# Kernel optimization log

Measured on AMD Instinct MI355X. Metric: run time of the kernel, lower is better.

Reference implementation:

```python
import jax, jax.numpy as jnp
import numpy as np

N_HEADS = 16
DIM_HEAD = 64
ROPE_THETA = 10000.0


def _rope_tables(seq_len, dim_head, dtype):
    # [N, dim_head//2] angle tables, llama-style interleaved-pair rotation
    inv_freq = 1.0 / (ROPE_THETA ** (jnp.arange(0, dim_head, 2, dtype=jnp.float32) / dim_head))
    t = jnp.arange(seq_len, dtype=jnp.float32)
    freqs = jnp.outer(t, inv_freq)  # [N, D/2]
    return jnp.cos(freqs).astype(dtype), jnp.sin(freqs).astype(dtype)


def _apply_rope(x, cos, sin):
    # x: [B, H, N, D]; rotate interleaved pairs (x[2i], x[2i+1])
    xr = x[..., 0::2]
    xi = x[..., 1::2]
    cos = cos[None, None, :, :]
    sin = sin[None, None, :, :]
    out_r = xr * cos - xi * sin
    out_i = xr * sin + xi * cos
    return jnp.stack([out_r, out_i], axis=-1).reshape(x.shape)


def _l2norm(x, eps=1e-12):
    return x / jnp.maximum(jnp.linalg.norm(x, axis=-1, keepdims=True), eps)


def setup_inputs() -> dict:
    key = jax.random.key(0)
    ks = jax.random.split(key, 5)
    B, N, dim = 1, 4096, N_HEADS * DIM_HEAD
    q = jax.random.normal(ks[0], (B, N, dim), dtype=jnp.float32)
    k = jax.random.normal(ks[1], (B, N, dim), dtype=jnp.float32)
    v = jax.random.normal(ks[2], (B, N, dim), dtype=jnp.float32)
    qk_scale = jnp.full((1, 1, 1, DIM_HEAD), 10.0, dtype=jnp.float32)
    w_out = jax.random.normal(ks[3], (dim, dim), dtype=jnp.float32) * (dim ** -0.5)
    b_out = jnp.zeros((dim,), dtype=jnp.float32)
    return {"q": q, "k": k, "v": v, "qk_scale": qk_scale, "w_out": w_out, "b_out": b_out}


def reference(q, k, v, qk_scale, w_out, b_out):
    B, N, dim = q.shape
    H, D = N_HEADS, DIM_HEAD
    scale = D ** -0.5
    # [B, N, dim] -> [B, H, N, D]
    q = q.reshape(B, N, H, D).transpose(0, 2, 1, 3)
    k = k.reshape(B, N, H, D).transpose(0, 2, 1, 3)
    v = v.reshape(B, N, H, D).transpose(0, 2, 1, 3)
    # RoPE
    cos, sin = _rope_tables(N, D, q.dtype)
    q = _apply_rope(q, cos, sin)
    k = _apply_rope(k, cos, sin)
    # QK-norm: L2-normalize then learned scale
    q = _l2norm(q) * qk_scale
    k = _l2norm(k) * qk_scale
    # explicit attention (non-flash)
    scores = jnp.einsum('bhid,bhjd->bhij', q, k) * scale
    probs = jax.nn.softmax(scores, axis=-1)
    out = jnp.einsum('bhij,bhjd->bhid', probs, v)
    out = out.transpose(0, 2, 1, 3).reshape(B, N, dim)
    # Linear: y = x W^T + b
    return out @ w_out.T + b_out
```

## Files before the change

kernel.cpp:

```cpp
#include <hip/hip_runtime.h>
#include <hip/hip_bf16.h>

#define N_CTX 4096
#define NH    16
#define DH    64
#define DIM   1024
#define NSPLIT 4
#define KT_PER_SPLIT (N_CTX / 64 / NSPLIT)

typedef __attribute__((ext_vector_type(8))) short bf16x8;
typedef __attribute__((ext_vector_type(4))) float f32x4;
typedef __attribute__((ext_vector_type(2))) unsigned u32x2;

__device__ __forceinline__ ushort f2bf(float f) {
    union { float f; unsigned u; } x; x.f = f;
    unsigned r = (x.u + 0x7FFFu + ((x.u >> 16) & 1u)) >> 16;
    return (ushort)r;
}
__device__ __forceinline__ float bf2f(ushort u) {
    union { unsigned u; float f; } x; x.u = ((unsigned)u) << 16; return x.f;
}
__device__ __forceinline__ unsigned fbits(float f) {
    union { float f; unsigned u; } x; x.f = f; return x.u;
}
__device__ __forceinline__ unsigned pack_bf16(float lo, float hi) {
    unsigned a = fbits(lo) + 0x8000u;
    unsigned b = fbits(hi) + 0x8000u;
#if defined(__has_builtin)
#if __has_builtin(__builtin_amdgcn_perm)
    return __builtin_amdgcn_perm(b, a, 0x07060302u);
#else
    return (a >> 16) | (b & 0xFFFF0000u);
#endif
#else
    return (a >> 16) | (b & 0xFFFF0000u);
#endif
}
__device__ __forceinline__ float fast_exp2(float x) {
#if defined(__has_builtin)
#if __has_builtin(__builtin_amdgcn_exp2f)
    return __builtin_amdgcn_exp2f(x);
#else
    return exp2f(x);
#endif
#else
    return exp2f(x);
#endif
}
__device__ __forceinline__ void fast_sincos(float ang, float* s, float* c) {
#if defined(__has_builtin)
#if __has_builtin(__builtin_amdgcn_sinf) && __has_builtin(__builtin_amdgcn_cosf) && __has_builtin(__builtin_amdgcn_fractf)
    float rev = __builtin_amdgcn_fractf(ang * 0.15915494309189535f);
    *s = __builtin_amdgcn_sinf(rev);
    *c = __builtin_amdgcn_cosf(rev);
    return;
#endif
#endif
    sincosf(ang, s, c);
}

__device__ __forceinline__ void pl32_swap(unsigned &a, unsigned &b) {
#if defined(__has_builtin)
#if __has_builtin(__builtin_amdgcn_permlane32_swap)
    u32x2 r = __builtin_amdgcn_permlane32_swap(a, b, false, false);
    a = r[0]; b = r[1];
    return;
#endif
#endif
    const int lane = (int)(threadIdx.x & 63);
    unsigned ax = (unsigned)__shfl_xor((int)a, 32, 64);
    unsigned bx = (unsigned)__shfl_xor((int)b, 32, 64);
    unsigned na = (lane & 32) ? bx : a;
    unsigned nb = (lane & 32) ? b  : ax;
    a = na; b = nb;
}
__device__ __forceinline__ void pl16_swap(unsigned &a, unsigned &b) {
#if defined(__has_builtin)
#if __has_builtin(__builtin_amdgcn_permlane16_swap)
    u32x2 r = __builtin_amdgcn_permlane16_swap(a, b, false, false);
    a = r[0]; b = r[1];
    return;
#endif
#endif
    const int lane = (int)(threadIdx.x & 63);
    unsigned ax = (unsigned)__shfl_xor((int)a, 16, 64);
    unsigned bx = (unsigned)__shfl_xor((int)b, 16, 64);
    unsigned na = (lane & 16) ? bx : a;
    unsigned nb = (lane & 16) ? b  : ax;
    a = na; b = nb;
}

#define SC 0.18033688011112042f
#define LF 0.4152410118609203f

__global__ __launch_bounds__(256) void prep_kernel(
    const float* __restrict__ qg, const float* __restrict__ kg,
    const float* __restrict__ qk_scale,
    ushort* __restrict__ qb, ushort* __restrict__ kb)
{
    const int lane = threadIdx.x & 63;
    const int wave = threadIdx.x >> 6;
    const int row  = blockIdx.x * 4 + wave;
    const int n = row >> 4;
    const int h = row & 15;
    const int isk = blockIdx.y;
    const float* __restrict__ x = isk ? kg : qg;
    ushort* __restrict__ xb = isk ? kb : qb;
    const float premul = isk ? 1.0f : SC;

    float val = x[(size_t)n * DIM + h * DH + lane];
    float other = __shfl_xor(val, 1, 64);

    const int i = lane >> 1;
    float inv_freq = fast_exp2((float)i * -LF);
    float ang = (float)n * inv_freq;
    float s, c;
    fast_sincos(ang, &s, &c);

    float r = (lane & 1) ? fmaf(other, s, val * c)
                         : fmaf(val, c, -(other * s));

    float ss = r * r;
    #pragma unroll
    for (int off = 32; off > 0; off >>= 1)
        ss += __shfl_xor(ss, off, 64);
    float invn = rsqrtf(fmaxf(ss, 1e-24f));
    float scl  = qk_scale[lane] * premul;

    xb[((size_t)h * N_CTX + n) * DH + lane] = f2bf(r * invn * scl);
}

__global__ __launch_bounds__(256) void vtrans_kernel(
    const float* __restrict__ v, ushort* __restrict__ vt)
{
    __shared__ ushort L[64][68];
    const int kt = blockIdx.x, h = blockIdx.y, t = threadIdx.x;

    for (int e = t; e < 4096; e += 256) {
        int key = e >> 6, d = e & 63;
        float f = v[(size_t)(kt * 64 + key) * DIM + h * DH + d];
        L[d][key] = f2bf(f);
    }
    __syncthreads();
    for (int e = t; e < 4096; e += 256) {
        int d = e >> 6, key = e & 63;
        vt[((size_t)h * DH + d) * N_CTX + kt * 64 + key] = L[d][key];
    }
}

__global__ __launch_bounds__(256) void wconv_kernel(
    const float* __restrict__ w, ushort* __restrict__ wb)
{
    int i = (blockIdx.x * 256 + threadIdx.x) * 4;
    float4 f = *(const float4*)&w[i];
    ushort4 u;
    u.x = f2bf(f.x); u.y = f2bf(f.y); u.z = f2bf(f.z); u.w = f2bf(f.w);
    *(ushort4*)&wb[i] = u;
}

__global__ __launch_bounds__(256) void attn_kernel(
    const ushort* __restrict__ qb, const ushort* __restrict__ kb,
    const ushort* __restrict__ vt, ushort* __restrict__ opart,
    float* __restrict__ lpart)
{
    __shared__ ushort Ks[2][64][72];
    __shared__ ushort Vt[2][64][72];

    const int h     = blockIdx.y;
    const int qbase = blockIdx.x * 128;
    const int sp    = blockIdx.z;
    const int kbase = sp * (N_CTX / NSPLIT);
    const int t    = threadIdx.x;
    const int w    = t >> 6;
    const int lane = t & 63;
    const int l15  = lane & 15;
    const int quad = lane >> 4;

    bf16x8 qf[2][2];
    #pragma unroll
    for (int qt = 0; qt < 2; qt++) {
        const size_t qrow = ((size_t)h * N_CTX + qbase + w * 32 + qt * 16 + l15) * DH;
        qf[qt][0] = *(const bf16x8*)&qb[qrow + quad * 8];
        qf[qt][1] = *(const bf16x8*)&qb[qrow + 32 + quad * 8];
    }

    float l_part[2] = {0.0f, 0.0f};
    f32x4 o_acc[4][2];
    #pragma unroll
    for (int dt = 0; dt < 4; dt++)
        #pragma unroll
        for (int qt = 0; qt < 2; qt++)
            o_acc[dt][qt] = (f32x4){0.f, 0.f, 0.f, 0.f};

    const int sr = t >> 3;
    const int sc = (t & 7) * 8;
    const ushort* kp0 = &kb[((size_t)h * N_CTX + kbase + sr) * DH + sc];
    const ushort* kp1 = kp0 + (size_t)32 * DH;
    const ushort* vp0 = &vt[((size_t)h * DH + sr) * N_CTX + kbase + sc];
    const ushort* vp1 = vp0 + (size_t)32 * N_CTX;

    bf16x8 kr0 = *(const bf16x8*)kp0, kr1 = *(const bf16x8*)kp1;
    bf16x8 vr0 = *(const bf16x8*)vp0, vr1 = *(const bf16x8*)vp1;
    kp0 += (size_t)64 * DH; kp1 += (size_t)64 * DH;
    vp0 += 64;              vp1 += 64;
    *(bf16x8*)&Ks[0][sr][sc]      = kr0;
    *(bf16x8*)&Ks[0][sr + 32][sc] = kr1;
    *(bf16x8*)&Vt[0][sr][sc]      = vr0;
    *(bf16x8*)&Vt[0][sr + 32][sc] = vr1;
    __syncthreads();

    for (int kt = 0; kt < KT_PER_SPLIT; kt++) {
        const int cur = kt & 1;
        const bool more = (kt + 1 < KT_PER_SPLIT);
        if (more) {
            kr0 = *(const bf16x8*)kp0;  kp0 += (size_t)64 * DH;
            kr1 = *(const bf16x8*)kp1;  kp1 += (size_t)64 * DH;
            vr0 = *(const bf16x8*)vp0;  vp0 += 64;
            vr1 = *(const bf16x8*)vp1;  vp1 += 64;
        }

        #pragma unroll
        for (int jp = 0; jp < 2; jp++) {
            unsigned pa[2][2], pb[2][2];
            #pragma unroll
            for (int jj = 0; jj < 2; jj++) {
                const int j = jp * 2 + jj;
                bf16x8 kf0 = *(const bf16x8*)&Ks[cur][j * 16 + l15][quad * 8];
                bf16x8 kf1 = *(const bf16x8*)&Ks[cur][j * 16 + l15][32 + quad * 8];
                f32x4 s0 = (f32x4){0.f, 0.f, 0.f, 0.f};
                f32x4 s1 = (f32x4){0.f, 0.f, 0.f, 0.f};
                s0 = __builtin_amdgcn_mfma_f32_16x16x32_bf16(kf0, qf[0][0], s0, 0, 0, 0);
                s1 = __builtin_amdgcn_mfma_f32_16x16x32_bf16(kf0, qf[1][0], s1, 0, 0, 0);
                s0 = __builtin_amdgcn_mfma_f32_16x16x32_bf16(kf1, qf[0][1], s0, 0, 0, 0);
                s1 = __builtin_amdgcn_mfma_f32_16x16x32_bf16(kf1, qf[1][1], s1, 0, 0, 0);

                {
                    float p0 = fast_exp2(s0.x), p1 = fast_exp2(s0.y);
                    float p2 = fast_exp2(s0.z), p3 = fast_exp2(s0.w);
                    l_part[0] += (p0 + p1) + (p2 + p3);
                    unsigned d0 = pack_bf16(p0, p1), d1 = pack_bf16(p2, p3);
                    if (jj == 0) { pa[0][0] = d0; pa[0][1] = d1; }
                    else         { pb[0][0] = d0; pb[0][1] = d1; }
                }
                {
                    float p0 = fast_exp2(s1.x), p1 = fast_exp2(s1.y);
                    float p2 = fast_exp2(s1.z), p3 = fast_exp2(s1.w);
                    l_part[1] += (p0 + p1) + (p2 + p3);
                    unsigned d0 = pack_bf16(p0, p1), d1 = pack_bf16(p2, p3);
                    if (jj == 0) { pa[1][0] = d0; pa[1][1] = d1; }
                    else         { pb[1][0] = d0; pb[1][1] = d1; }
                }
            }

            bf16x8 pw[2];
            #pragma unroll
            for (int qt = 0; qt < 2; qt++) {
                unsigned x0 = pa[qt][0], y0 = pb[qt][0];
                unsigned x1 = pa[qt][1], y1 = pb[qt][1];
                pl32_swap(x0, y0);
                pl32_swap(x1, y1);
                pl16_swap(x0, y0);
                pl16_swap(x1, y1);
                uint4 wd; wd.x = x0; wd.y = x1; wd.z = y0; wd.w = y1;
                pw[qt] = __builtin_bit_cast(bf16x8, wd);
            }

            #pragma unroll
            for (int dt = 0; dt < 4; dt++) {
                bf16x8 vf = *(const bf16x8*)&Vt[cur][dt * 16 + l15][jp * 32 + quad * 8];
                o_acc[dt][0] = __builtin_amdgcn_mfma_f32_16x16x32_bf16(vf, pw[0], o_acc[dt][0], 0, 0, 0);
                o_acc[dt][1] = __builtin_amdgcn_mfma_f32_16x16x32_bf16(vf, pw[1], o_acc[dt][1], 0, 0, 0);
            }
        }

        if (more) {
            *(bf16x8*)&Ks[cur ^ 1][sr][sc]      = kr0;
            *(bf16x8*)&Ks[cur ^ 1][sr + 32][sc] = kr1;
            *(bf16x8*)&Vt[cur ^ 1][sr][sc]      = vr0;
            *(bf16x8*)&Vt[cur ^ 1][sr + 32][sc] = vr1;
            __syncthreads();
        }
    }

    #pragma unroll
    for (int qt = 0; qt < 2; qt++) {
        float v = l_part[qt];
        v += __shfl_xor(v, 16, 64);
        v += __shfl_xor(v, 32, 64);
        if (quad == 0)
            lpart[(size_t)sp * NH * N_CTX + (size_t)h * N_CTX
                  + qbase + w * 32 + qt * 16 + l15] = v;
    }

    #pragma unroll
    for (int qt = 0; qt < 2; qt++)
        #pragma unroll
        for (int dt = 0; dt < 4; dt++) {
            f32x4 o = o_acc[dt][qt];
            ushort4 ov;
            ov.x = f2bf(o.x); ov.y = f2bf(o.y);
            ov.z = f2bf(o.z); ov.w = f2bf(o.w);
            *(ushort4*)&opart[((size_t)sp * N_CTX + qbase + w * 32 + qt * 16 + l15) * DIM
                              + h * DH + dt * 16 + quad * 4] = ov;
        }
}

__global__ __launch_bounds__(256) void combine_kernel(
    const ushort* __restrict__ opart, const float* __restrict__ lpart,
    ushort* __restrict__ attnb)
{
    const int idx = blockIdx.x * 256 + threadIdx.x;
    const int n   = idx >> 8;
    const int rem = idx & 255;
    const int h   = rem >> 4;
    const size_t e = (size_t)n * DIM + h * DH + (rem & 15) * 4;

    float s0 = 0.f, s1 = 0.f, s2 = 0.f, s3 = 0.f, lsum = 0.f;
    #pragma unroll
    for (int sp = 0; sp < NSPLIT; sp++) {
        ushort4 u = *(const ushort4*)&opart[(size_t)sp * N_CTX * DIM + e];
        s0 += bf2f(u.x); s1 += bf2f(u.y); s2 += bf2f(u.z); s3 += bf2f(u.w);
        lsum += lpart[(size_t)sp * NH * N_CTX + (size_t)h * N_CTX + n];
    }
    float li = 1.0f / lsum;

    ushort4 r;
    r.x = f2bf(s0 * li); r.y = f2bf(s1 * li);
    r.z = f2bf(s2 * li); r.w = f2bf(s3 * li);
    *(ushort4*)&attnb[e] = r;
}

__global__ __launch_bounds__(256) void proj_kernel(
    const ushort* __restrict__ A, const ushort* __restrict__ W,
    const float* __restrict__ bias, float* __restrict__ out)
{
    __shared__ ushort As[2][64][72];
    __shared__ ushort Ws[2][64][72];

    const int nbase = blockIdx.x * 64;
    const int obase = blockIdx.y * 64;
    const int t    = threadIdx.x;
    const int w    = t >> 6;
    const int lane = t & 63;
    const int l15  = lane & 15;
    const int quad = lane >> 4;
    const int rw   = (w >> 1) * 32;
    const int cw   = (w & 1) * 32;

    f32x4 acc[2][2];
    #pragma unroll
    for (int mt = 0; mt < 2; mt++)
        #pragma unroll
        for (int nt = 0; nt < 2; nt++)
            acc[mt][nt] = (f32x4){0.f, 0.f, 0.f, 0.f};

    const int sr = t >> 3;
    const int sc = (t & 7) * 8;
    const ushort* ap0 = &A[(size_t)(nbase + sr) * DIM + sc];
    const ushort* ap1 = ap0 + (size_t)32 * DIM;
    const ushort* wp0 = &W[(size_t)(obase + sr) * DIM + sc];
    const ushort* wp1 = wp0 + (size_t)32 * DIM;

    bf16x8 ar0 = *(const bf16x8*)ap0, ar1 = *(const bf16x8*)ap1;
    bf16x8 wr0 = *(const bf16x8*)wp0, wr1 = *(const bf16x8*)wp1;
    ap0 += 64; ap1 += 64; wp0 += 64; wp1 += 64;
    *(bf16x8*)&As[0][sr][sc]      = ar0;
    *(bf16x8*)&As[0][sr + 32][sc] = ar1;
    *(bf16x8*)&Ws[0][sr][sc]      = wr0;
    *(bf16x8*)&Ws[0][sr + 32][sc] = wr1;
    __syncthreads();

    for (int kt = 0; kt < DIM / 64; kt++) {
        const int cur = kt & 1;
        const bool more = (kt + 1 < DIM / 64);
        if (more) {
            ar0 = *(const bf16x8*)ap0;  ap0 += 64;
            ar1 = *(const bf16x8*)ap1;  ap1 += 64;
            wr0 = *(const bf16x8*)wp0;  wp0 += 64;
            wr1 = *(const bf16x8*)wp1;  wp1 += 64;
        }

        bf16x8 af[2][2], bfr[2][2];
        #pragma unroll
        for (int mt = 0; mt < 2; mt++)
            #pragma unroll
            for (int kh = 0; kh < 2; kh++)
                af[mt][kh] = *(const bf16x8*)&As[cur][rw + mt * 16 + l15][kh * 32 + quad * 8];
        #pragma unroll
        for (int nt = 0; nt < 2; nt++)
            #pragma unroll
            for (int kh = 0; kh < 2; kh++)
                bfr[nt][kh] = *(const bf16x8*)&Ws[cur][cw + nt * 16 + l15][kh * 32 + quad * 8];

        #pragma unroll
        for (int mt = 0; mt < 2; mt++)
            #pragma unroll
            for (int nt = 0; nt < 2; nt++) {
                acc[mt][nt] = __builtin_amdgcn_mfma_f32_16x16x32_bf16(af[mt][0], bfr[nt][0], acc[mt][nt], 0, 0, 0);
                acc[mt][nt] = __builtin_amdgcn_mfma_f32_16x16x32_bf16(af[mt][1], bfr[nt][1], acc[mt][nt], 0, 0, 0);
            }

        if (more) {
            *(bf16x8*)&As[cur ^ 1][sr][sc]      = ar0;
            *(bf16x8*)&As[cur ^ 1][sr + 32][sc] = ar1;
            *(bf16x8*)&Ws[cur ^ 1][sr][sc]      = wr0;
            *(bf16x8*)&Ws[cur ^ 1][sr + 32][sc] = wr1;
            __syncthreads();
        }
    }

    #pragma unroll
    for (int nt = 0; nt < 2; nt++) {
        int o = obase + cw + nt * 16 + l15;
        float bb = bias[o];
        #pragma unroll
        for (int mt = 0; mt < 2; mt++) {
            int nrow = nbase + rw + mt * 16 + quad * 4;
            out[(size_t)(nrow + 0) * DIM + o] = acc[mt][nt].x + bb;
            out[(size_t)(nrow + 1) * DIM + o] = acc[mt][nt].y + bb;
            out[(size_t)(nrow + 2) * DIM + o] = acc[mt][nt].z + bb;
            out[(size_t)(nrow + 3) * DIM + o] = acc[mt][nt].w + bb;
        }
    }
}

extern "C" void kernel_launch(void* const* d_in, const int* in_sizes, int n_in,
                              void* d_out, int out_size, void* d_ws, size_t ws_size,
                              hipStream_t stream)
{
    const float* q        = (const float*)d_in[0];
    const float* k        = (const float*)d_in[1];
    const float* v        = (const float*)d_in[2];
    const float* qk_scale = (const float*)d_in[3];
    const float* w_out    = (const float*)d_in[4];
    const float* b_out    = (const float*)d_in[5];
    float* out = (float*)d_out;

    const size_t per = (size_t)NH * N_CTX * DH;
    ushort* qb    = (ushort*)d_ws;
    ushort* kb    = qb + per;
    ushort* vtg   = kb + per;
    ushort* attnb = vtg + per;
    ushort* wb    = attnb + per;
    ushort* opart = wb + (size_t)DIM * DIM;
    float*  lpart = (float*)(opart + (size_t)NSPLIT * N_CTX * DIM);

    prep_kernel<<<dim3(N_CTX * NH / 4, 2), 256, 0, stream>>>(q, k, qk_scale, qb, kb);
    vtrans_kernel<<<dim3(N_CTX / 64, NH), 256, 0, stream>>>(v, vtg);
    wconv_kernel<<<dim3(DIM * DIM / 1024), 256, 0, stream>>>(w_out, wb);
    attn_kernel<<<dim3(N_CTX / 128, NH, NSPLIT), 256, 0, stream>>>(qb, kb, vtg, opart, lpart);
    combine_kernel<<<dim3(N_CTX * DIM / 4 / 256), 256, 0, stream>>>(opart, lpart, attnb);
    proj_kernel<<<dim3(N_CTX / 64, DIM / 64), 256, 0, stream>>>(attnb, wb, b_out, out);
}
```

Measured before the change: 241.0 us.

## Double attention Q tile per block, single-buffer K/V smem, precompute RoPE tables

```diff
diff --git a/kernel.cpp b/kernel.cpp
--- a/kernel.cpp
+++ b/kernel.cpp
@@ -93,9 +93,21 @@
 #define SC 0.18033688011112042f
 #define LF 0.4152410118609203f
 
+__global__ __launch_bounds__(256) void rope_table_kernel(
+    float* __restrict__ ct, float* __restrict__ st)
+{
+    const int idx = blockIdx.x * 256 + threadIdx.x;
+    const int n = idx >> 5, i = idx & 31;
+    float inv_freq = fast_exp2((float)i * -LF);
+    float s, c;
+    fast_sincos((float)n * inv_freq, &s, &c);
+    ct[idx] = c; st[idx] = s;
+}
+
 __global__ __launch_bounds__(256) void prep_kernel(
     const float* __restrict__ qg, const float* __restrict__ kg,
     const float* __restrict__ qk_scale,
+    const float* __restrict__ ct, const float* __restrict__ st,
     ushort* __restrict__ qb, ushort* __restrict__ kb)
 {
     const int lane = threadIdx.x & 63;
@@ -112,10 +124,8 @@
     float other = __shfl_xor(val, 1, 64);
 
     const int i = lane >> 1;
-    float inv_freq = fast_exp2((float)i * -LF);
-    float ang = (float)n * inv_freq;
-    float s, c;
-    fast_sincos(ang, &s, &c);
+    const float c = ct[(n << 5) | i];
+    const float s = st[(n << 5) | i];
 
     float r = (lane & 1) ? fmaf(other, s, val * c)
                          : fmaf(val, c, -(other * s));
@@ -163,11 +173,11 @@
     const ushort* __restrict__ vt, ushort* __restrict__ opart,
     float* __restrict__ lpart)
 {
-    __shared__ ushort Ks[2][64][72];
-    __shared__ ushort Vt[2][64][72];
+    __shared__ ushort Ks[64][72];
+    __shared__ ushort Vt[64][72];
 
     const int h     = blockIdx.y;
-    const int qbase = blockIdx.x * 128;
+    const int qbase = blockIdx.x * 256;
     const int sp    = blockIdx.z;
     const int kbase = sp * (N_CTX / NSPLIT);
     const int t    = threadIdx.x;
@@ -176,20 +186,20 @@
     const int l15  = lane & 15;
     const int quad = lane >> 4;
 
-    bf16x8 qf[2][2];
-    #pragma unroll
-    for (int qt = 0; qt < 2; qt++) {
-        const size_t qrow = ((size_t)h * N_CTX + qbase + w * 32 + qt * 16 + l15) * DH;
+    bf16x8 qf[4][2];
+    #pragma unroll
+    for (int qt = 0; qt < 4; qt++) {
+        const size_t qrow = ((size_t)h * N_CTX + qbase + w * 64 + qt * 16 + l15) * DH;
         qf[qt][0] = *(const bf16x8*)&qb[qrow + quad * 8];
         qf[qt][1] = *(const bf16x8*)&qb[qrow + 32 + quad * 8];
     }
 
-    float l_part[2] = {0.0f, 0.0f};
-    f32x4 o_acc[4][2];
+    float l_part[4] = {0.f, 0.f, 0.f, 0.f};
+    f32x4 o_acc[4][4];
     #pragma unroll
     for (int dt = 0; dt < 4; dt++)
         #pragma unroll
-        for (int qt = 0; qt < 2; qt++)
+        for (int qt = 0; qt < 4; qt++)
             o_acc[dt][qt] = (f32x4){0.f, 0.f, 0.f, 0.f};
 
     const int sr = t >> 3;
@@ -198,63 +208,56 @@
     const ushort* kp1 = kp0 + (size_t)32 * DH;
     const ushort* vp0 = &vt[((size_t)h * DH + sr) * N_CTX + kbase + sc];
     const ushort* vp1 = vp0 + (size_t)32 * N_CTX;
-
     bf16x8 kr0 = *(const bf16x8*)kp0, kr1 = *(const bf16x8*)kp1;
     bf16x8 vr0 = *(const bf16x8*)vp0, vr1 = *(const bf16x8*)vp1;
-    kp0 += (size_t)64 * DH; kp1 += (size_t)64 * DH;
-    vp0 += 64;              vp1 += 64;
-    *(bf16x8*)&Ks[0][sr][sc]      = kr0;
-    *(bf16x8*)&Ks[0][sr + 32][sc] = kr1;
-    *(bf16x8*)&Vt[0][sr][sc]      = vr0;
-    *(bf16x8*)&Vt[0][sr + 32][sc] = vr1;
-    __syncthreads();
 
     for (int kt = 0; kt < KT_PER_SPLIT; kt++) {
-        const int cur = kt & 1;
-        const bool more = (kt + 1 < KT_PER_SPLIT);
-        if (more) {
-            kr0 = *(const bf16x8*)kp0;  kp0 += (size_t)64 * DH;
-            kr1 = *(const bf16x8*)kp1;  kp1 += (size_t)64 * DH;
-            vr0 = *(const bf16x8*)vp0;  vp0 += 64;
-            vr1 = *(const bf16x8*)vp1;  vp1 += 64;
+        __syncthreads();
+        *(bf16x8*)&Ks[sr][sc]      = kr0;
+        *(bf16x8*)&Ks[sr + 32][sc] = kr1;
+        *(bf16x8*)&Vt[sr][sc]      = vr0;
+        *(bf16x8*)&Vt[sr + 32][sc] = vr1;
+        __syncthreads();
+        if (kt + 1 < KT_PER_SPLIT) {
+            kr0 = *(const bf16x8*)(kp0 + (size_t)(kt + 1) * 64 * DH);
+            kr1 = *(const bf16x8*)(kp1 + (size_t)(kt + 1) * 64 * DH);
+            vr0 = *(const bf16x8*)(vp0 + (size_t)(kt + 1) * 64);
+            vr1 = *(const bf16x8*)(vp1 + (size_t)(kt + 1) * 64);
         }
 
         #pragma unroll
         for (int jp = 0; jp < 2; jp++) {
-            unsigned pa[2][2], pb[2][2];
+            unsigned pa[4][2], pb[4][2];
             #pragma unroll
             for (int jj = 0; jj < 2; jj++) {
                 const int j = jp * 2 + jj;
-                bf16x8 kf0 = *(const bf16x8*)&Ks[cur][j * 16 + l15][quad * 8];
-                bf16x8 kf1 = *(const bf16x8*)&Ks[cur][j * 16 + l15][32 + quad * 8];
-                f32x4 s0 = (f32x4){0.f, 0.f, 0.f, 0.f};
-                f32x4 s1 = (f32x4){0.f, 0.f, 0.f, 0.f};
-                s0 = __builtin_amdgcn_mfma_f32_16x16x32_bf16(kf0, qf[0][0], s0, 0, 0, 0);
-                s1 = __builtin_amdgcn_mfma_f32_16x16x32_bf16(kf0, qf[1][0], s1, 0, 0, 0);
-                s0 = __builtin_amdgcn_mfma_f32_16x16x32_bf16(kf1, qf[0][1], s0, 0, 0, 0);
-                s1 = __builtin_amdgcn_mfma_f32_16x16x32_bf16(kf1, qf[1][1], s1, 0, 0, 0);
-
-                {
-                    float p0 = fast_exp2(s0.x), p1 = fast_exp2(s0.y);
-                    float p2 = fast_exp2(s0.z), p3 = fast_exp2(s0.w);
-                    l_part[0] += (p0 + p1) + (p2 + p3);
+                bf16x8 kf0 = *(const bf16x8*)&Ks[j * 16 + l15][quad * 8];
+                bf16x8 kf1 = *(const bf16x8*)&Ks[j * 16 + l15][32 + quad * 8];
+                f32x4 sv[4];
+                #pragma unroll
+                for (int qt = 0; qt < 4; qt++)
+                    sv[qt] = (f32x4){0.f, 0.f, 0.f, 0.f};
+                #pragma unroll
+                for (int qt = 0; qt < 4; qt++)
+                    sv[qt] = __builtin_amdgcn_mfma_f32_16x16x32_bf16(kf0, qf[qt][0], sv[qt], 0, 0, 0);
+                #pragma unroll
+                for (int qt = 0; qt < 4; qt++)
+                    sv[qt] = __builtin_amdgcn_mfma_f32_16x16x32_bf16(kf1, qf[qt][1], sv[qt], 0, 0, 0);
+
+                #pragma unroll
+                for (int qt = 0; qt < 4; qt++) {
+                    float p0 = fast_exp2(sv[qt].x), p1 = fast_exp2(sv[qt].y);
+                    float p2 = fast_exp2(sv[qt].z), p3 = fast_exp2(sv[qt].w);
+                    l_part[qt] += (p0 + p1) + (p2 + p3);
                     unsigned d0 = pack_bf16(p0, p1), d1 = pack_bf16(p2, p3);
-                    if (jj == 0) { pa[0][0] = d0; pa[0][1] = d1; }
-                    else         { pb[0][0] = d0; pb[0][1] = d1; }
-                }
-                {
-                    float p0 = fast_exp2(s1.x), p1 = fast_exp2(s1.y);
-                    float p2 = fast_exp2(s1.z), p3 = fast_exp2(s1.w);
-                    l_part[1] += (p0 + p1) + (p2 + p3);
-                    unsigned d0 = pack_bf16(p0, p1), d1 = pack_bf16(p2, p3);
-                    if (jj == 0) { pa[1][0] = d0; pa[1][1] = d1; }
-                    else         { pb[1][0] = d0; pb[1][1] = d1; }
+                    if (jj == 0) { pa[qt][0] = d0; pa[qt][1] = d1; }
+                    else         { pb[qt][0] = d0; pb[qt][1] = d1; }
                 }
             }
 
-            bf16x8 pw[2];
-            #pragma unroll
-            for (int qt = 0; qt < 2; qt++) {
+            bf16x8 pw[4];
+            #pragma unroll
+            for (int qt = 0; qt < 4; qt++) {
                 unsigned x0 = pa[qt][0], y0 = pb[qt][0];
                 unsigned x1 = pa[qt][1], y1 = pb[qt][1];
                 pl32_swap(x0, y0);
@@ -267,40 +270,33 @@
 
             #pragma unroll
             for (int dt = 0; dt < 4; dt++) {
-                bf16x8 vf = *(const bf16x8*)&Vt[cur][dt * 16 + l15][jp * 32 + quad * 8];
-                o_acc[dt][0] = __builtin_amdgcn_mfma_f32_16x16x32_bf16(vf, pw[0], o_acc[dt][0], 0, 0, 0);
-                o_acc[dt][1] = __builtin_amdgcn_mfma_f32_16x16x32_bf16(vf, pw[1], o_acc[dt][1], 0, 0, 0);
+                bf16x8 vf = *(const bf16x8*)&Vt[dt * 16 + l15][jp * 32 + quad * 8];
+                #pragma unroll
+                for (int qt = 0; qt < 4; qt++)
+                    o_acc[dt][qt] = __builtin_amdgcn_mfma_f32_16x16x32_bf16(vf, pw[qt], o_acc[dt][qt], 0, 0, 0);
             }
         }
-
-        if (more) {
-            *(bf16x8*)&Ks[cur ^ 1][sr][sc]      = kr0;
-            *(bf16x8*)&Ks[cur ^ 1][sr + 32][sc] = kr1;
-            *(bf16x8*)&Vt[cur ^ 1][sr][sc]      = vr0;
-            *(bf16x8*)&Vt[cur ^ 1][sr + 32][sc] = vr1;
-            __syncthreads();
-        }
-    }
-
-    #pragma unroll
-    for (int qt = 0; qt < 2; qt++) {
+    }
+
+    #pragma unroll
+    for (int qt = 0; qt < 4; qt++) {
         float v = l_part[qt];
         v += __shfl_xor(v, 16, 64);
         v += __shfl_xor(v, 32, 64);
         if (quad == 0)
             lpart[(size_t)sp * NH * N_CTX + (size_t)h * N_CTX
-                  + qbase + w * 32 + qt * 16 + l15] = v;
-    }
-
-    #pragma unroll
-    for (int qt = 0; qt < 2; qt++)
+                  + qbase + w * 64 + qt * 16 + l15] = v;
+    }
+
+    #pragma unroll
+    for (int qt = 0; qt < 4; qt++)
         #pragma unroll
         for (int dt = 0; dt < 4; dt++) {
             f32x4 o = o_acc[dt][qt];
             ushort4 ov;
             ov.x = f2bf(o.x); ov.y = f2bf(o.y);
             ov.z = f2bf(o.z); ov.w = f2bf(o.w);
-            *(ushort4*)&opart[((size_t)sp * N_CTX + qbase + w * 32 + qt * 16 + l15) * DIM
+            *(ushort4*)&opart[((size_t)sp * N_CTX + qbase + w * 64 + qt * 16 + l15) * DIM
                               + h * DH + dt * 16 + quad * 4] = ov;
         }
 }
@@ -444,11 +440,14 @@
     ushort* wb    = attnb + per;
     ushort* opart = wb + (size_t)DIM * DIM;
     float*  lpart = (float*)(opart + (size_t)NSPLIT * N_CTX * DIM);
-
-    prep_kernel<<<dim3(N_CTX * NH / 4, 2), 256, 0, stream>>>(q, k, qk_scale, qb, kb);
+    float*  ct    = lpart + (size_t)NSPLIT * NH * N_CTX;
+    float*  st    = ct + (size_t)N_CTX * 32;
+
+    rope_table_kernel<<<dim3(N_CTX * 32 / 256), 256, 0, stream>>>(ct, st);
+    prep_kernel<<<dim3(N_CTX * NH / 4, 2), 256, 0, stream>>>(q, k, qk_scale, ct, st, qb, kb);
     vtrans_kernel<<<dim3(N_CTX / 64, NH), 256, 0, stream>>>(v, vtg);
     wconv_kernel<<<dim3(DIM * DIM / 1024), 256, 0, stream>>>(w_out, wb);
-    attn_kernel<<<dim3(N_CTX / 128, NH, NSPLIT), 256, 0, stream>>>(qb, kb, vtg, opart, lpart);
+    attn_kernel<<<dim3(N_CTX / 256, NH, NSPLIT), 256, 0, stream>>>(qb, kb, vtg, opart, lpart);
     combine_kernel<<<dim3(N_CTX * DIM / 4 / 256), 256, 0, stream>>>(opart, lpart, attnb);
     proj_kernel<<<dim3(N_CTX / 64, DIM / 64), 256, 0, stream>>>(attnb, wb, b_out, out);
 }
```

Result: no change. 238.3 us (-1.1%).
